# Optimization experiments

Measured on AMD Instinct MI355X. Metric: run time of the kernel, lower is better.

Reference implementation:

```python
import jax, jax.numpy as jnp
import numpy as np

N_HEAD = 16


def setup_inputs() -> dict:
    key = jax.random.key(0)
    ks = jax.random.split(key, 12)
    B, T, S, D = 64, 1, 448, 1024
    x = jax.random.normal(ks[0], (B, T, D), dtype=jnp.float32)
    k_cache = jax.random.normal(ks[1], (B, S, D), dtype=jnp.float32)
    v_cache = jax.random.normal(ks[2], (B, S, D), dtype=jnp.float32)
    current_index = jax.random.randint(ks[3], (1,), 0, S, dtype=jnp.int64)
    attention_mask = jnp.zeros((1, S), dtype=jnp.float32)
    s = 0.02
    Wq = jax.random.normal(ks[4], (D, D), dtype=jnp.float32) * s
    bq = jax.random.normal(ks[5], (D,), dtype=jnp.float32) * s
    Wk = jax.random.normal(ks[6], (D, D), dtype=jnp.float32) * s  # whisper key proj has no bias
    Wv = jax.random.normal(ks[7], (D, D), dtype=jnp.float32) * s
    bv = jax.random.normal(ks[8], (D,), dtype=jnp.float32) * s
    Wo = jax.random.normal(ks[9], (D, D), dtype=jnp.float32) * s
    bo = jax.random.normal(ks[10], (D,), dtype=jnp.float32) * s
    return {"x": x, "k_cache": k_cache, "v_cache": v_cache,
            "current_index": current_index, "attention_mask": attention_mask,
            "Wq": Wq, "bq": bq, "Wk": Wk, "Wv": Wv, "bv": bv, "Wo": Wo, "bo": bo}


def reference(x, k_cache, v_cache, current_index, attention_mask,
              Wq, bq, Wk, Wv, bv, Wo, bo):
    B, T, D = x.shape            # T == 1 (single decode token)
    S = k_cache.shape[1]         # cache length (448)
    H = N_HEAD
    Dh = D // H
    scale = float(Dh) ** -0.25

    # q/k/v projections of the new token
    q = x @ Wq + bq              # [B, T, D]
    k = x @ Wk                   # [B, T, D]
    v = x @ Wv + bv              # [B, T, D]

    # scatter the new token into the caches at current_index (functional clone+write)
    idx = current_index[0]
    k_upd = jax.lax.dynamic_update_slice(k_cache, k, (0, idx, 0))  # [B, S, D]
    v_upd = jax.lax.dynamic_update_slice(v_cache, v, (0, idx, 0))

    # whisper qkv_attention: scale q and k each by Dh**-0.25
    qh = q.reshape(B, T, H, Dh).transpose(0, 2, 1, 3) * scale      # [B, H, T, Dh]
    kh = k_upd.reshape(B, S, H, Dh).transpose(0, 2, 3, 1) * scale  # [B, H, Dh, S]
    vh = v_upd.reshape(B, S, H, Dh).transpose(0, 2, 1, 3)          # [B, H, S, Dh]

    qk = qh @ kh + attention_mask          # [B, H, T, S]  (mask broadcasts)
    w = jax.nn.softmax(qk, axis=-1)
    wv = (w @ vh).transpose(0, 2, 1, 3).reshape(B, T, D)

    out = wv @ Wo + bo
    return out, k_upd, v_upd
```

## Files before the change

### kernel.cpp

```cpp
#include <hip/hip_runtime.h>

#define B_SZ    64
#define S_LEN   448
#define D_MODEL 1024
#define N_HEAD  16
#define D_HEAD  64
#define CHUNK   28
#define NCH     16
#define PF      8

typedef float f4 __attribute__((ext_vector_type(4)));

__global__ __launch_bounds__(256) void gemm_part(
    const float* __restrict__ X,
    const float* __restrict__ W0, const float* __restrict__ W1,
    const float* __restrict__ W2,
    float* __restrict__ P)
{
    const int nt  = blockIdx.x;
    const int kt  = blockIdx.y;
    const int mat = blockIdx.z;
    const float* __restrict__ W = (mat == 0) ? W0 : ((mat == 1) ? W1 : W2);

    const int t  = threadIdx.x;
    const int n  = nt * 64 + (t & 63);
    const int b0 = __builtin_amdgcn_readfirstlane((t >> 6) * 16);
    const int k0 = kt * 128;

    float acc[16];
#pragma unroll
    for (int j = 0; j < 16; ++j) acc[j] = 0.f;

#pragma unroll 8
    for (int k = k0; k < k0 + 128; ++k) {
        const float w = W[k * D_MODEL + n];
#pragma unroll
        for (int j = 0; j < 16; ++j)
            acc[j] += X[(b0 + j) * D_MODEL + k] * w;
    }

    float* p = P + (size_t)(mat * 8 + kt) * (B_SZ * D_MODEL);
#pragma unroll
    for (int j = 0; j < 16; ++j)
        p[(b0 + j) * D_MODEL + n] = acc[j];
}

__global__ __launch_bounds__(256) void reduce_out(
    const float* __restrict__ P, const float* __restrict__ bo,
    float* __restrict__ out)
{
    const int i = blockIdx.x * 256 + threadIdx.x;
    float s = bo[i & (D_MODEL - 1)];
#pragma unroll
    for (int kt = 0; kt < 8; ++kt)
        s += P[(size_t)kt * 65536 + i];
    out[i] = s;
}

__global__ __launch_bounds__(256) void stream_attn(
    const float* __restrict__ kcache, const float* __restrict__ vcache,
    const float* __restrict__ part,
    const float* __restrict__ bq, const float* __restrict__ bv,
    const float* __restrict__ amask, const int* __restrict__ idxp,
    float* __restrict__ kout, float* __restrict__ vout,
    float* __restrict__ accws, float* __restrict__ mlws)
{
    const int c   = blockIdx.x;
    const int b   = blockIdx.y;
    const int t   = threadIdx.x;
    const int col = t * 4;
    const int h   = t >> 4;
    const int l16 = t & 15;
    const int idx = idxp[0];
    const int s0  = c * CHUNK;

    f4 q = *(const f4*)(bq + col);
#pragma unroll
    for (int kt = 0; kt < 8; ++kt)
        q += *(const f4*)(part + (size_t)kt * 65536 + b * D_MODEL + col);

    f4 knew = (f4)0.f, vnew = (f4)0.f;
    const bool hasidx = (idx >= s0) && (idx < s0 + CHUNK);
    if (hasidx) {
#pragma unroll
        for (int kt = 0; kt < 8; ++kt) {
            knew += *(const f4*)(part + (size_t)(8 + kt)  * 65536 + b * D_MODEL + col);
            vnew += *(const f4*)(part + (size_t)(16 + kt) * 65536 + b * D_MODEL + col);
        }
        vnew += *(const f4*)(bv + col);
    }

    const size_t base = (size_t)(b * S_LEN + s0) * D_MODEL + col;

    f4 kb[PF], vb[PF];
#pragma unroll
    for (int r = 0; r < PF; ++r) {
        kb[r] = *(const f4*)(kcache + base + (size_t)r * D_MODEL);
        vb[r] = *(const f4*)(vcache + base + (size_t)r * D_MODEL);
    }

    float m = -1e30f, l = 0.f;
    f4 acc = (f4)0.f;

#pragma unroll
    for (int s = 0; s < CHUNK; ++s) {
        f4 k4 = kb[s & (PF - 1)];
        f4 v4 = vb[s & (PF - 1)];
        if (s + PF < CHUNK) {
            kb[s & (PF - 1)] = *(const f4*)(kcache + base + (size_t)(s + PF) * D_MODEL);
            vb[s & (PF - 1)] = *(const f4*)(vcache + base + (size_t)(s + PF) * D_MODEL);
        }
        const int srow = s0 + s;
        if (srow == idx) { k4 = knew; v4 = vnew; }
        const size_t roff = base + (size_t)s * D_MODEL;
        __builtin_nontemporal_store(k4, (f4*)(kout + roff));
        __builtin_nontemporal_store(v4, (f4*)(vout + roff));

        float p = q.x * k4.x + q.y * k4.y + q.z * k4.z + q.w * k4.w;
        p += __shfl_xor(p, 1);
        p += __shfl_xor(p, 2);
        p += __shfl_xor(p, 4);
        p += __shfl_xor(p, 8);
        p = p * 0.125f + amask[srow];

        const float mn = fmaxf(m, p);
        const float f  = __expf(m - mn);
        const float w  = __expf(p - mn);
        l = l * f + w;
        acc.x = acc.x * f + w * v4.x;
        acc.y = acc.y * f + w * v4.y;
        acc.z = acc.z * f + w * v4.z;
        acc.w = acc.w * f + w * v4.w;
        m = mn;
    }

    float* ap = accws + ((size_t)(b * N_HEAD + h) * NCH + c) * D_HEAD + l16 * 4;
    *(f4*)ap = acc;
    if (l16 == 0) {
        const int w = (b * N_HEAD + h) * NCH + c;
        mlws[w * 2]     = m;
        mlws[w * 2 + 1] = l;
    }
}

__global__ __launch_bounds__(256) void combine(
    const float* __restrict__ accws, const float* __restrict__ mlws,
    float* __restrict__ wvws)
{
    const int t = threadIdx.x;
    const int w = blockIdx.x * 4 + (t >> 6);
    const int d = t & 63;

    float M = -1e30f;
#pragma unroll
    for (int c = 0; c < NCH; ++c)
        M = fmaxf(M, mlws[(w * NCH + c) * 2]);
    float L = 0.f, O = 0.f;
#pragma unroll
    for (int c = 0; c < NCH; ++c) {
        const float f = __expf(mlws[(w * NCH + c) * 2] - M);
        L += mlws[(w * NCH + c) * 2 + 1] * f;
        O += accws[(w * NCH + c) * D_HEAD + d] * f;
    }
    const int b = w >> 4, h = w & 15;
    wvws[b * D_MODEL + h * D_HEAD + d] = O / L;
}

extern "C" void kernel_launch(void* const* d_in, const int* in_sizes, int n_in,
                              void* d_out, int out_size, void* d_ws, size_t ws_size,
                              hipStream_t stream) {
    const float* x      = (const float*)d_in[0];
    const float* kcache = (const float*)d_in[1];
    const float* vcache = (const float*)d_in[2];
    const int*   idxp   = (const int*)d_in[3];
    const float* amask  = (const float*)d_in[4];
    const float* Wq     = (const float*)d_in[5];
    const float* bq     = (const float*)d_in[6];
    const float* Wk     = (const float*)d_in[7];
    const float* Wv     = (const float*)d_in[8];
    const float* bv     = (const float*)d_in[9];
    const float* Wo     = (const float*)d_in[10];
    const float* bo     = (const float*)d_in[11];

    float* out  = (float*)d_out;
    float* kout = out + 65536;
    float* vout = kout + (size_t)B_SZ * S_LEN * D_MODEL;

    float* ws    = (float*)d_ws;
    float* part  = ws;
    float* accws = ws + 1572864;
    float* mlws  = ws + 2621440;
    float* wvws  = ws + 2654208;

    gemm_part<<<dim3(16, 8, 3), 256, 0, stream>>>(x, Wq, Wk, Wv, part);

    stream_attn<<<dim3(NCH, B_SZ), 256, 0, stream>>>(
        kcache, vcache, part, bq, bv, amask, idxp,
        kout, vout, accws, mlws);

    combine<<<256, 256, 0, stream>>>(accws, mlws, wvws);

    gemm_part<<<dim3(16, 8, 1), 256, 0, stream>>>(wvws, Wo, Wo, Wo, part);
    reduce_out<<<256, 256, 0, stream>>>(part, bo, out);
}
```

Measured before the change: 160.2 us.

## Split KV cache copy out of attention into separate streaming copy kernel

The attention kernel no longer writes the updated K/V caches. A grid-stride `cache_copy` kernel now copies both caches with nontemporal stores, and a small `kv_fix` kernel then writes the new token row at the current index. The aim is to let the attention pass stream reads only and the copy run as a simple bandwidth-bound loop. In exchange, the K/V caches are read from memory twice instead of once, which adds a large amount of traffic.

```diff
diff --git a/kernel.cpp b/kernel.cpp
--- a/kernel.cpp
+++ b/kernel.cpp
@@ -8,6 +8,7 @@
 #define CHUNK   28
 #define NCH     16
 #define PF      8
+#define CPY_BLK 2048
 
 typedef float f4 __attribute__((ext_vector_type(4)));
 
@@ -57,12 +58,11 @@
     out[i] = s;
 }
 
-__global__ __launch_bounds__(256) void stream_attn(
+__global__ __launch_bounds__(256) void attn_read(
     const float* __restrict__ kcache, const float* __restrict__ vcache,
     const float* __restrict__ part,
     const float* __restrict__ bq, const float* __restrict__ bv,
     const float* __restrict__ amask, const int* __restrict__ idxp,
-    float* __restrict__ kout, float* __restrict__ vout,
     float* __restrict__ accws, float* __restrict__ mlws)
 {
     const int c   = blockIdx.x;
@@ -80,8 +80,7 @@
         q += *(const f4*)(part + (size_t)kt * 65536 + b * D_MODEL + col);
 
     f4 knew = (f4)0.f, vnew = (f4)0.f;
-    const bool hasidx = (idx >= s0) && (idx < s0 + CHUNK);
-    if (hasidx) {
+    if ((idx >= s0) && (idx < s0 + CHUNK)) {
 #pragma unroll
         for (int kt = 0; kt < 8; ++kt) {
             knew += *(const f4*)(part + (size_t)(8 + kt)  * 65536 + b * D_MODEL + col);
@@ -112,9 +111,6 @@
         }
         const int srow = s0 + s;
         if (srow == idx) { k4 = knew; v4 = vnew; }
-        const size_t roff = base + (size_t)s * D_MODEL;
-        __builtin_nontemporal_store(k4, (f4*)(kout + roff));
-        __builtin_nontemporal_store(v4, (f4*)(vout + roff));
 
         float p = q.x * k4.x + q.y * k4.y + q.z * k4.z + q.w * k4.w;
         p += __shfl_xor(p, 1);
@@ -141,6 +137,44 @@
         mlws[w * 2]     = m;
         mlws[w * 2 + 1] = l;
     }
+}
+
+__global__ __launch_bounds__(256) void cache_copy(
+    const float* __restrict__ kcache, const float* __restrict__ vcache,
+    float* __restrict__ kout, float* __restrict__ vout)
+{
+    const size_t n4     = (size_t)B_SZ * S_LEN * D_MODEL / 4;
+    const size_t stride = (size_t)CPY_BLK * 256;
+    const f4* __restrict__ ks = (const f4*)kcache;
+    const f4* __restrict__ vs = (const f4*)vcache;
+    f4* __restrict__ kd = (f4*)kout;
+    f4* __restrict__ vd = (f4*)vout;
+    size_t i = (size_t)blockIdx.x * 256 + threadIdx.x;
+#pragma unroll 7
+    for (; i < n4; i += stride) {
+        __builtin_nontemporal_store(ks[i], kd + i);
+        __builtin_nontemporal_store(vs[i], vd + i);
+    }
+}
+
+__global__ __launch_bounds__(256) void kv_fix(
+    const float* __restrict__ part, const float* __restrict__ bv,
+    const int* __restrict__ idxp,
+    float* __restrict__ kout, float* __restrict__ vout)
+{
+    const int b   = blockIdx.x;
+    const int col = threadIdx.x * 4;
+    const int idx = idxp[0];
+    f4 kn = (f4)0.f, vn = (f4)0.f;
+#pragma unroll
+    for (int kt = 0; kt < 8; ++kt) {
+        kn += *(const f4*)(part + (size_t)(8 + kt)  * 65536 + b * D_MODEL + col);
+        vn += *(const f4*)(part + (size_t)(16 + kt) * 65536 + b * D_MODEL + col);
+    }
+    vn += *(const f4*)(bv + col);
+    const size_t roff = (size_t)(b * S_LEN + idx) * D_MODEL + col;
+    *(f4*)(kout + roff) = kn;
+    *(f4*)(vout + roff) = vn;
 }
 
 __global__ __launch_bounds__(256) void combine(
@@ -194,12 +228,14 @@
 
     gemm_part<<<dim3(16, 8, 3), 256, 0, stream>>>(x, Wq, Wk, Wv, part);
 
-    stream_attn<<<dim3(NCH, B_SZ), 256, 0, stream>>>(
-        kcache, vcache, part, bq, bv, amask, idxp,
-        kout, vout, accws, mlws);
+    attn_read<<<dim3(NCH, B_SZ), 256, 0, stream>>>(
+        kcache, vcache, part, bq, bv, amask, idxp, accws, mlws);
 
     combine<<<256, 256, 0, stream>>>(accws, mlws, wvws);
 
     gemm_part<<<dim3(16, 8, 1), 256, 0, stream>>>(wvws, Wo, Wo, Wo, part);
     reduce_out<<<256, 256, 0, stream>>>(part, bo, out);
-}
+
+    cache_copy<<<CPY_BLK, 256, 0, stream>>>(kcache, vcache, kout, vout);
+    kv_fix<<<B_SZ, 256, 0, stream>>>(part, bv, idxp, kout, vout);
+}
```

Result: slower. 200.4 us (+25.1%).
